# Performance work log

Hardware: AMD Instinct MI355X
Metric: run time of the kernel (lower is better)

The kernel has to match this reference:

```python
import jax, jax.numpy as jnp
import numpy as np

EMB = 2048
NH = 16
HD = EMB // NH  # 128

def setup_inputs() -> dict:
    key = jax.random.key(0)
    kx, kw1, kw2 = jax.random.split(key, 3)
    T = 4096
    x = jax.random.normal(kx, (T, EMB), dtype=jnp.float32)
    lim_in = 1.0 / np.sqrt(EMB)
    # input_proj: Linear(EMB, 3*EMB, use_bias=False), weight shape (out, in)
    W_in = jax.random.uniform(kw1, (3 * EMB, EMB), minval=-lim_in, maxval=lim_in, dtype=jnp.float32)
    W_out = jax.random.uniform(kw2, (EMB, EMB), minval=-lim_in, maxval=lim_in, dtype=jnp.float32)
    return {"x": x, "W_in": W_in, "W_out": W_out}

def reference(x, W_in, W_out):
    T = x.shape[0]
    norm = 1.0 / np.sqrt(HD)
    qkv = x @ W_in.T                         # [T, 3E]
    Q, K, V = jnp.split(qkv, 3, axis=-1)     # each [T, E]
    Q = Q.reshape(T, NH, HD).transpose(1, 0, 2)  # [nh, T, hd]
    K = K.reshape(T, NH, HD).transpose(1, 0, 2)
    V = V.reshape(T, NH, HD).transpose(1, 0, 2)
    A = jnp.einsum('htd,hsd->hts', Q, K) * norm  # [nh, T, T]
    mask = jnp.tri(T, dtype=bool)                # causal: keep lower triangle
    A = jnp.where(mask, A, -jnp.inf)
    P = jax.nn.softmax(A, axis=-1)
    y = jnp.einsum('hts,hsd->htd', P, V)         # [nh, T, hd]
    y = y.transpose(1, 0, 2).reshape(T, EMB)     # concat heads
    return y @ W_out.T
```

## Files before the change

### kernel.cpp

```cpp
#include <hip/hip_runtime.h>
#include <hip/hip_bf16.h>
#include <cstddef>


typedef __attribute__((ext_vector_type(8))) short short8;
typedef __attribute__((ext_vector_type(4))) float f32x4;

#define MFMA16(a, b, c) __builtin_amdgcn_mfma_f32_16x16x32_bf16((a), (b), (c), 0, 0, 0)

#define GLOAD_LDS16(gptr, lptr)                                                          \
  __builtin_amdgcn_global_load_lds((const __attribute__((address_space(1))) void*)(gptr), \
                                   (__attribute__((address_space(3))) void*)(lptr), 16, 0, 0)

#define PSWZ(q) ((((q) & 7) ^ ((q) >> 3)) << 3)

__device__ __forceinline__ short f2bf(float f) {
  __hip_bfloat16 h = __float2bfloat16(f);
  return *reinterpret_cast<short*>(&h);
}

__device__ __forceinline__ void storeC(float* p, float v) { *p = v; }
__device__ __forceinline__ void storeC(short* p, float v) { *p = f2bf(v); }

__global__ void cvt_bf16(const float* __restrict__ in, short* __restrict__ out,
                         long n, float scale, long scaleN) {
  long i = ((long)blockIdx.x * 256 + threadIdx.x) * 8;
  if (i >= n) return;
  float s = (i < scaleN) ? scale : 1.0f;
  f32x4 a = *(const f32x4*)(in + i);
  f32x4 b = *(const f32x4*)(in + i + 4);
  short8 o;
  o[0] = f2bf(a[0] * s); o[1] = f2bf(a[1] * s); o[2] = f2bf(a[2] * s); o[3] = f2bf(a[3] * s);
  o[4] = f2bf(b[0] * s); o[5] = f2bf(b[1] * s); o[6] = f2bf(b[2] * s); o[7] = f2bf(b[3] * s);
  *(short8*)(out + i) = o;
}

template <typename CT>
__global__ __launch_bounds__(256, 4)
void gemm_bt(const short* __restrict__ A, const short* __restrict__ B,
             CT* __restrict__ C, int M, int N, int K) {
  __shared__ short As[128 * 64];
  __shared__ short Bs[128 * 64];
  const int tid = threadIdx.x;
  const int wave = tid >> 6, lane = tid & 63;
  const int g = lane >> 4, fr = lane & 15;
  const int wr = (wave >> 1) * 64, wc = (wave & 1) * 64;
  const int bm = blockIdx.y * 128, bn = blockIdx.x * 128;

  f32x4 acc[4][4] = {};

  for (int k0 = 0; k0 < K; k0 += 64) {
    __syncthreads();
#pragma unroll
    for (int i = 0; i < 4; ++i) {
      int Ci = i * 256 + tid;
      int row = Ci >> 3, c = Ci & 7;
      int sc = c ^ (row & 7);
      GLOAD_LDS16(A + (size_t)(bm + row) * K + k0 + sc * 8, As + Ci * 8);
      GLOAD_LDS16(B + (size_t)(bn + row) * K + k0 + sc * 8, Bs + Ci * 8);
    }
    __syncthreads();

#pragma unroll
    for (int kk = 0; kk < 2; ++kk) {
      short8 af[4], bfr[4];
#pragma unroll
      for (int m = 0; m < 4; ++m) {
        int row = wr + m * 16 + fr;
        int off = (kk * 32 + g * 8) ^ ((row & 7) * 8);
        af[m] = *(const short8*)(As + row * 64 + off);
      }
#pragma unroll
      for (int n = 0; n < 4; ++n) {
        int row = wc + n * 16 + fr;
        int off = (kk * 32 + g * 8) ^ ((row & 7) * 8);
        bfr[n] = *(const short8*)(Bs + row * 64 + off);
      }
#pragma unroll
      for (int m = 0; m < 4; ++m)
#pragma unroll
        for (int n = 0; n < 4; ++n)
          acc[m][n] = MFMA16(af[m], bfr[n], acc[m][n]);
    }
  }

#pragma unroll
  for (int m = 0; m < 4; ++m) {
#pragma unroll
    for (int r = 0; r < 4; ++r) {
      size_t row = (size_t)(bm + wr + m * 16 + g * 4 + r);
      CT* cp = C + row * N + bn + wc + fr;
#pragma unroll
      for (int n = 0; n < 4; ++n)
        storeC(cp + n * 16, acc[m][n][r]);
    }
  }
}

__global__ __launch_bounds__(256, 4)
void vtrans(const short* __restrict__ qkv, short* __restrict__ vtg) {
  __shared__ short L[128 * 64];
  const int tid = threadIdx.x;
  const int tb = blockIdx.x * 64;
  const int h = blockIdx.y;
#pragma unroll
  for (int i = 0; i < 4; ++i) {
    int Ci = i * 256 + tid, tok = Ci >> 4, c = Ci & 15, f0 = c * 8;
    short8 v = *(const short8*)(qkv + (size_t)(tb + tok) * 6144 + 4096 + h * 128 + f0);
#pragma unroll
    for (int j = 0; j < 8; ++j) {
      int f = f0 + j;
      L[f * 64 + (tok ^ ((((f & 7) ^ ((f >> 3) & 7)) << 3)))] = v[j];
    }
  }
  __syncthreads();
  const int f = tid >> 1, half = (tid & 1) * 32;
  const int s_in = ((f & 7) ^ ((f >> 3) & 7)) << 3;
  const int s_out = (f & 7) << 3;
#pragma unroll
  for (int j2 = 0; j2 < 4; ++j2) {
    int t0 = half + j2 * 8;
    short8 v = *(const short8*)(&L[f * 64 + (t0 ^ s_in)]);
    *(short8*)(vtg + (size_t)(h * 128 + f) * 4096 + tb + (t0 ^ s_out)) = v;
  }
}

__global__ __launch_bounds__(256, 2)
void attn_fwd(const short* __restrict__ qkv, const short* __restrict__ vtg,
              short* __restrict__ y) {
  __shared__ short Ks[2][64 * 128];
  __shared__ short Vt[128 * 64];
  __shared__ short Ps[4][32 * 64];
  const int tid = threadIdx.x;
  const int wave = tid >> 6, lane = tid & 63;
  const int g = lane >> 4, fr = lane & 15;

  const int wgid = blockIdx.x;
  const int xcd = wgid & 7, mid = (wgid >> 3) & 31, slot = wgid >> 8;
  const int h = (xcd << 1) | (mid & 1);
  const int xq = mid >> 1;
  const int x = slot ? xq : 31 - xq;
  const int qw = x * 128 + wave * 32;
  const int ntiles = 2 * x + 2;

  short* Pw = Ps[wave];

  short8 onesf;
#pragma unroll
  for (int j = 0; j < 8; ++j) onesf[j] = (short)0x3F80;

  short8 qf[2][4];
#pragma unroll
  for (int mi = 0; mi < 2; ++mi) {
    const short* Qp = qkv + (size_t)(qw + mi * 16 + fr) * 6144 + h * 128;
#pragma unroll
    for (int kk = 0; kk < 4; ++kk)
      qf[mi][kk] = *(const short8*)(Qp + kk * 32 + g * 8);
  }
  f32x4 oacc[2][8] = {};
  f32x4 lacc[2] = {};

#pragma unroll
  for (int i = 0; i < 4; ++i) {
    int Ci = i * 256 + tid, key = Ci >> 4, c = Ci & 15, sc = c ^ (key & 7);
    GLOAD_LDS16(qkv + (size_t)key * 6144 + 2048 + h * 128 + sc * 8, &Ks[0][Ci * 8]);
  }
#pragma unroll
  for (int i = 0; i < 4; ++i) {
    int Ci = i * 256 + tid, feat = Ci >> 3, ko = (Ci & 7) * 8;
    GLOAD_LDS16(vtg + (size_t)(h * 128 + feat) * 4096 + ko, &Vt[Ci * 8]);
  }
  __syncthreads();

#pragma unroll 1
  for (int t = 0; t < ntiles; ++t) {
    const int kv0 = t * 64;
    const int cur = t & 1;

    if (t > 0) {
#pragma unroll
      for (int i = 0; i < 4; ++i) {
        int Ci = i * 256 + tid, feat = Ci >> 3, ko = (Ci & 7) * 8;
        GLOAD_LDS16(vtg + (size_t)(h * 128 + feat) * 4096 + kv0 + ko, &Vt[Ci * 8]);
      }
    }
    if (t + 1 < ntiles) {
#pragma unroll
      for (int i = 0; i < 4; ++i) {
        int Ci = i * 256 + tid, key = Ci >> 4, c = Ci & 15, sc = c ^ (key & 7);
        GLOAD_LDS16(qkv + (size_t)(kv0 + 64 + key) * 6144 + 2048 + h * 128 + sc * 8,
                    &Ks[cur ^ 1][Ci * 8]);
      }
    }

    const bool active = (kv0 <= qw + 31);

    if (active) {
      f32x4 s[2][4] = {};
      __builtin_amdgcn_s_setprio(1);
#pragma unroll
      for (int nf = 0; nf < 4; ++nf) {
        const int key = nf * 16 + fr;
#pragma unroll
        for (int kk = 0; kk < 4; ++kk) {
          int off = (kk * 32 + g * 8) ^ ((key & 7) * 8);
          short8 kfrag = *(const short8*)(&Ks[cur][key * 128 + off]);
          s[0][nf] = MFMA16(qf[0][kk], kfrag, s[0][nf]);
          s[1][nf] = MFMA16(qf[1][kk], kfrag, s[1][nf]);
        }
      }
      __builtin_amdgcn_s_setprio(0);

      if (t >= ntiles - 2) {
#pragma unroll
        for (int mi = 0; mi < 2; ++mi)
#pragma unroll
          for (int nf = 0; nf < 4; ++nf) {
            const int keyg = kv0 + nf * 16 + fr;
#pragma unroll
            for (int r = 0; r < 4; ++r) {
              const int q2 = mi * 16 + g * 4 + r;
              float p = (keyg <= qw + q2) ? __builtin_amdgcn_exp2f(s[mi][nf][r]) : 0.f;
              Pw[q2 * 64 + ((nf * 16 + fr) ^ PSWZ(q2))] = f2bf(p);
            }
          }
      } else {
#pragma unroll
        for (int mi = 0; mi < 2; ++mi)
#pragma unroll
          for (int nf = 0; nf < 4; ++nf)
#pragma unroll
            for (int r = 0; r < 4; ++r) {
              const int q2 = mi * 16 + g * 4 + r;
              Pw[q2 * 64 + ((nf * 16 + fr) ^ PSWZ(q2))] =
                  f2bf(__builtin_amdgcn_exp2f(s[mi][nf][r]));
            }
      }
    }

    __syncthreads();

    if (active) {
      __builtin_amdgcn_s_setprio(1);
#pragma unroll
      for (int kk = 0; kk < 2; ++kk) {
        const int rb = kk * 32 + g * 8;
        short8 pf0 = *(const short8*)(&Pw[fr * 64 + (rb ^ PSWZ(fr))]);
        short8 pf1 = *(const short8*)(&Pw[(16 + fr) * 64 + (rb ^ PSWZ(16 + fr))]);
        lacc[0] = MFMA16(pf0, onesf, lacc[0]);
        lacc[1] = MFMA16(pf1, onesf, lacc[1]);
#pragma unroll
        for (int nf = 0; nf < 8; ++nf) {
          int f = nf * 16 + fr;
          short8 vf = *(const short8*)(&Vt[f * 64 + (rb ^ ((f & 7) * 8))]);
          oacc[0][nf] = MFMA16(pf0, vf, oacc[0][nf]);
          oacc[1][nf] = MFMA16(pf1, vf, oacc[1][nf]);
        }
      }
      __builtin_amdgcn_s_setprio(0);
    }

    __syncthreads();
  }

#pragma unroll
  for (int mi = 0; mi < 2; ++mi)
#pragma unroll
    for (int r = 0; r < 4; ++r) {
      float inv = 1.0f / lacc[mi][r];
      size_t row = (size_t)(qw + mi * 16 + g * 4 + r);
#pragma unroll
      for (int nf = 0; nf < 8; ++nf)
        y[row * 2048 + h * 128 + nf * 16 + fr] = f2bf(oacc[mi][nf][r] * inv);
    }
}

extern "C" void kernel_launch(void* const* d_in, const int* in_sizes, int n_in,
                              void* d_out, int out_size, void* d_ws, size_t ws_size,
                              hipStream_t stream) {
  const float* x    = (const float*)d_in[0];
  const float* Win  = (const float*)d_in[1];
  const float* Wout = (const float*)d_in[2];
  float* out = (float*)d_out;

  char* ws = (char*)d_ws;
  short* xb    = (short*)(ws);
  short* yb    = (short*)(ws);
  short* Winb  = (short*)(ws + 16777216);
  short* vtg   = (short*)(ws + 16777216);
  short* Woutb = (short*)(ws + 41943040);
  short* qkv   = (short*)(ws + 50331648);

  const float qscale = 0.08838834764831845f * 1.4426950408889634f;

  cvt_bf16<<<4096, 256, 0, stream>>>(x, xb, 8388608L, 1.0f, 0L);
  cvt_bf16<<<6144, 256, 0, stream>>>(Win, Winb, 12582912L, qscale, 4194304L);
  cvt_bf16<<<2048, 256, 0, stream>>>(Wout, Woutb, 4194304L, 1.0f, 0L);

  gemm_bt<short><<<dim3(48, 32), 256, 0, stream>>>(xb, Winb, qkv, 4096, 6144, 2048);

  vtrans<<<dim3(64, 16), 256, 0, stream>>>(qkv, vtg);

  attn_fwd<<<512, 256, 0, stream>>>(qkv, vtg, yb);

  gemm_bt<float><<<dim3(16, 32), 256, 0, stream>>>(yb, Woutb, out, 4096, 2048, 2048);
}
```

Before: 284.2 us.

## Use 256x256 double-buffered GEMM tile for QKV projection

Adds a new GEMM kernel with 256x256 output tiles, 512 threads, double-buffered LDS staging via direct global-to-LDS loads, and a block-index swizzle that groups blocks for cache locality. It is used only for the QKV input projection. The goal is more operand reuse per tile and overlap of the next tile's loads with MFMA work. The cost is 128KB of LDS per block, which limits occupancy, and a grid of 384 blocks that may fill the CUs unevenly.

```diff
diff --git a/kernel.cpp b/kernel.cpp
--- a/kernel.cpp
+++ b/kernel.cpp
@@ -36,6 +36,100 @@
 }
 
 template <typename CT>
+__global__ __launch_bounds__(512, 2)
+void gemm_bt256(const short* __restrict__ A, const short* __restrict__ B,
+                CT* __restrict__ C, int M, int N, int K) {
+  __shared__ short As[2][256 * 64];
+  __shared__ short Bs[2][256 * 64];
+  const int tid = threadIdx.x;
+  const int lane = tid & 63, wave = tid >> 6;
+  const int g = lane >> 4, fr = lane & 15;
+  const int wm = wave >> 2, wn = wave & 3;
+
+  const int cpx = gridDim.x >> 3;
+  const int sw = ((int)blockIdx.x & 7) * cpx + ((int)blockIdx.x >> 3);
+  const int bxn = N >> 8;
+  const int bm = (sw / bxn) * 256, bn = (sw % bxn) * 256;
+
+  const int nkt = K >> 6;
+
+#define STAGE256(buf, kt)                                                       \
+  do {                                                                          \
+    const int k0_ = (kt) << 6;                                                  \
+    _Pragma("unroll") for (int i = 0; i < 4; ++i) {                             \
+      int Ci = i * 512 + tid;                                                   \
+      int row = Ci >> 3, c = Ci & 7, sc = c ^ (row & 7);                        \
+      GLOAD_LDS16(A + (size_t)(bm + row) * K + k0_ + sc * 8, &As[buf][Ci * 8]); \
+    }                                                                           \
+    _Pragma("unroll") for (int i = 0; i < 4; ++i) {                             \
+      int Ci = i * 512 + tid;                                                   \
+      int row = Ci >> 3, c = Ci & 7, sc = c ^ (row & 7);                        \
+      GLOAD_LDS16(B + (size_t)(bn + row) * K + k0_ + sc * 8, &Bs[buf][Ci * 8]); \
+    }                                                                           \
+  } while (0)
+
+  f32x4 acc[8][4] = {};
+
+  STAGE256(0, 0);
+  STAGE256(1, 1);
+  asm volatile("s_waitcnt vmcnt(8)" ::: "memory");
+  __builtin_amdgcn_s_barrier();
+
+  for (int kt = 0; kt < nkt; ++kt) {
+    const int cur = kt & 1;
+    const short* Ap = As[cur];
+    const short* Bp = Bs[cur];
+
+    __builtin_amdgcn_s_setprio(1);
+#pragma unroll
+    for (int kk = 0; kk < 2; ++kk) {
+      short8 af[8], bf[4];
+#pragma unroll
+      for (int m = 0; m < 8; ++m) {
+        int row = wm * 128 + m * 16 + fr;
+        int off = ((kk * 4 + g) ^ (row & 7)) * 8;
+        af[m] = *(const short8*)(Ap + row * 64 + off);
+      }
+#pragma unroll
+      for (int n = 0; n < 4; ++n) {
+        int row = wn * 64 + n * 16 + fr;
+        int off = ((kk * 4 + g) ^ (row & 7)) * 8;
+        bf[n] = *(const short8*)(Bp + row * 64 + off);
+      }
+#pragma unroll
+      for (int m = 0; m < 8; ++m)
+#pragma unroll
+        for (int n = 0; n < 4; ++n)
+          acc[m][n] = MFMA16(af[m], bf[n], acc[m][n]);
+    }
+    __builtin_amdgcn_s_setprio(0);
+
+    if (kt + 2 < nkt) {
+      __builtin_amdgcn_s_barrier();
+      STAGE256(cur, kt + 2);
+      asm volatile("s_waitcnt vmcnt(8)" ::: "memory");
+      __builtin_amdgcn_s_barrier();
+    } else if (kt + 1 < nkt) {
+      asm volatile("s_waitcnt vmcnt(0)" ::: "memory");
+      __builtin_amdgcn_s_barrier();
+    }
+  }
+#undef STAGE256
+
+#pragma unroll
+  for (int m = 0; m < 8; ++m) {
+#pragma unroll
+    for (int r = 0; r < 4; ++r) {
+      size_t row = (size_t)(bm + wm * 128 + m * 16 + g * 4 + r);
+      CT* cp = C + row * N + bn + wn * 64 + fr;
+#pragma unroll
+      for (int n = 0; n < 4; ++n)
+        storeC(cp + n * 16, acc[m][n][r]);
+    }
+  }
+}
+
+template <typename CT>
 __global__ __launch_bounds__(256, 4)
 void gemm_bt(const short* __restrict__ A, const short* __restrict__ B,
              CT* __restrict__ C, int M, int N, int K) {
@@ -297,7 +391,7 @@
   cvt_bf16<<<6144, 256, 0, stream>>>(Win, Winb, 12582912L, qscale, 4194304L);
   cvt_bf16<<<2048, 256, 0, stream>>>(Wout, Woutb, 4194304L, 1.0f, 0L);
 
-  gemm_bt<short><<<dim3(48, 32), 256, 0, stream>>>(xb, Winb, qkv, 4096, 6144, 2048);
+  gemm_bt256<short><<<384, 512, 0, stream>>>(xb, Winb, qkv, 4096, 6144, 2048);
 
   vtrans<<<dim3(64, 16), 256, 0, stream>>>(qkv, vtg);
 
```

Result: slower. 311.2 us (+9.5%).
